# Optimization experiments

Measured on AMD Instinct MI355X. Metric: run time of the kernel, lower is better.

## Reference

```python
import jax, jax.numpy as jnp
import numpy as np

WINDOW = 5
SIGMA = 4.0
KSIZE = 2 * int(4.0 * SIGMA + 0.5) + 1  # 33, matches torchvision GaussianBlur setup

H1, W1, B, N, C = 56, 56, 16, 32, 512
PAD = WINDOW - 1


def _gauss_kernel():
    x = jnp.arange(KSIZE, dtype=jnp.float32) - (KSIZE - 1) / 2.0
    k = jnp.exp(-0.5 * (x / SIGMA) ** 2)
    return k / jnp.sum(k)


def _blur(img):
    # separable Gaussian blur with reflect padding (torchvision GaussianBlur default)
    k = _gauss_kernel()
    p = KSIZE // 2
    x = jnp.pad(img, ((0, 0), (0, 0), (p, p), (p, p)), mode='reflect')
    dn = ('NCHW', 'OIHW', 'NCHW')
    x = jax.lax.conv_general_dilated(x, k.reshape(1, 1, KSIZE, 1), (1, 1), 'VALID', dimension_numbers=dn)
    x = jax.lax.conv_general_dilated(x, k.reshape(1, 1, 1, KSIZE), (1, 1), 'VALID', dimension_numbers=dn)
    return x


def _forward(embeddings, memory_bank, out_h, out_w):
    H, W, Bb, Cc = embeddings.shape
    x_norm = jnp.sum(embeddings * embeddings, axis=-1, keepdims=True)  # H W B 1
    best = None
    for d1 in range(WINDOW):
        for d2 in range(WINDOW):
            y = memory_bank[d1:H + d1, d2:W + d2]            # H W N C (shifted slice)
            y_norm = jnp.sum(y * y, axis=-1)                  # H W N
            cross = jnp.einsum('hwbc,hwnc->hwbn', embeddings, y)
            dsq = jnp.maximum(x_norm - 2.0 * cross + y_norm[:, :, None, :], 0.0)
            dmin = jnp.sqrt(jnp.min(dsq, axis=-1))            # H W B
            best = dmin if best is None else jnp.minimum(best, dmin)
    pix = jnp.transpose(best, (2, 0, 1))[:, None, :, :]        # B 1 H W
    img = jnp.max(pix, axis=(1, 2, 3))                         # B
    pix = jax.image.resize(pix, (Bb, 1, out_h, out_w), method='linear')  # align_corners=False bilinear
    return img, _blur(pix)


def setup_inputs() -> dict:
    key = jax.random.key(0)
    k1, k2 = jax.random.split(key)
    embeddings = jax.random.normal(k1, (H1, W1, B, C), dtype=jnp.float32)
    memory_bank = jax.random.normal(k2, (H1 + PAD, W1 + PAD, N, C), dtype=jnp.float32)
    return {'embeddings': embeddings, 'memory_bank': memory_bank, 'out_h': 224, 'out_w': 224}


def reference(embeddings, memory_bank, out_h, out_w):
    return _forward(embeddings, memory_bank, out_h, out_w)
```

## Files before the change

### kernel.cpp

```cpp
#include <hip/hip_runtime.h>
#include <math.h>

#define H1 56
#define W1 56
#define BB 16
#define NN 32
#define CC 512
#define MH 60
#define MW 60
#define OH 224
#define OW 224

typedef __bf16 bf16x8 __attribute__((ext_vector_type(8)));
typedef float floatx4 __attribute__((ext_vector_type(4)));

#define MBH_OFF    0
#define F_YN_OFF   29491200
#define F_BEST_OFF 29606400
#define F_TMP1_OFF 29656576
#define F_TOTAL_FLOATS 29857280ull

#define S_XN_OFF   0
#define S_YN_OFF   50176
#define S_BEST_OFF 165376
#define S_TMP1_OFF 215552

#define GLOAD_LDS16(g, l) __builtin_amdgcn_global_load_lds( \
    (const __attribute__((address_space(1))) unsigned int*)(g), \
    (__attribute__((address_space(3))) unsigned int*)(l), 16, 0, 0)

__global__ void cvt_norm_kernel(const float* __restrict__ src, __bf16* __restrict__ dsth,
                                float* __restrict__ norm, int nvec) {
    int wid  = (int)((blockIdx.x * blockDim.x + threadIdx.x) >> 6);
    int lane = threadIdx.x & 63;
    if (wid >= nvec) return;
    const float* p = src + (size_t)wid * CC + lane * 8;
    floatx4 a = *(const floatx4*)p;
    floatx4 b = *(const floatx4*)(p + 4);
    if (dsth) {
        bf16x8 v;
        v[0] = (__bf16)a.x; v[1] = (__bf16)a.y; v[2] = (__bf16)a.z; v[3] = (__bf16)a.w;
        v[4] = (__bf16)b.x; v[5] = (__bf16)b.y; v[6] = (__bf16)b.z; v[7] = (__bf16)b.w;
        *(bf16x8*)(dsth + (size_t)wid * CC + lane * 8) = v;
    }
    float s = a.x*a.x + a.y*a.y + a.z*a.z + a.w*a.w
            + b.x*b.x + b.y*b.y + b.z*b.z + b.w*b.w;
    s += __shfl_xor(s, 32, 64);
    s += __shfl_xor(s, 16, 64);
    s += __shfl_xor(s, 8, 64);
    s += __shfl_xor(s, 4, 64);
    s += __shfl_xor(s, 2, 64);
    s += __shfl_xor(s, 1, 64);
    if (lane == 0) norm[wid] = s;
}

#define BSTRIDE 520

__global__ __launch_bounds__(256, 2) void dist_kernel_bf16(
        const float* __restrict__ emb, const __bf16* __restrict__ mbh,
        const float* __restrict__ ynorm, float* __restrict__ best) {
    __shared__ __bf16 Bs[2][NN * BSTRIDE];

    int bx0  = blockIdx.x;
    int bx   = (bx0 & 7) * 49 + (bx0 >> 3);
    int h0   = (bx / 14) * 2;
    int w0   = (bx % 14) * 4;
    int tid  = threadIdx.x;
    int wave = tid >> 6;
    int lane = tid & 63;
    int nrow = lane & 15;
    int seg  = lane >> 4;
    int w    = w0 + wave;

    bf16x8 afragA[16], afragB[16];
    float snA = 0.f, snB = 0.f;
    const float* apA = emb + ((size_t)(h0 * W1 + w) * BB + nrow) * CC + seg * 8;
    const float* apB = apA + (size_t)W1 * BB * CC;
#pragma unroll
    for (int kk = 0; kk < 16; kk++) {
        floatx4 a0 = *(const floatx4*)(apA + kk * 32);
        floatx4 a1 = *(const floatx4*)(apA + kk * 32 + 4);
        floatx4 b0 = *(const floatx4*)(apB + kk * 32);
        floatx4 b1 = *(const floatx4*)(apB + kk * 32 + 4);
        bf16x8 va, vb;
        va[0] = (__bf16)a0.x; va[1] = (__bf16)a0.y; va[2] = (__bf16)a0.z; va[3] = (__bf16)a0.w;
        va[4] = (__bf16)a1.x; va[5] = (__bf16)a1.y; va[6] = (__bf16)a1.z; va[7] = (__bf16)a1.w;
        vb[0] = (__bf16)b0.x; vb[1] = (__bf16)b0.y; vb[2] = (__bf16)b0.z; vb[3] = (__bf16)b0.w;
        vb[4] = (__bf16)b1.x; vb[5] = (__bf16)b1.y; vb[6] = (__bf16)b1.z; vb[7] = (__bf16)b1.w;
        afragA[kk] = va; afragB[kk] = vb;
        snA += a0.x*a0.x + a0.y*a0.y + a0.z*a0.z + a0.w*a0.w
             + a1.x*a1.x + a1.y*a1.y + a1.z*a1.z + a1.w*a1.w;
        snB += b0.x*b0.x + b0.y*b0.y + b0.z*b0.z + b0.w*b0.w
             + b1.x*b1.x + b1.y*b1.y + b1.z*b1.z + b1.w*b1.w;
    }
    snA += __shfl_xor(snA, 16, 64); snA += __shfl_xor(snA, 32, 64);
    snB += __shfl_xor(snB, 16, 64); snB += __shfl_xor(snB, 32, 64);
    floatx4 xnA, xnB;
#pragma unroll
    for (int r = 0; r < 4; r++) {
        xnA[r] = __shfl(snA, seg * 4 + r, 64);
        xnB[r] = __shfl(snB, seg * 4 + r, 64);
    }

    float bvA[4] = {1e30f, 1e30f, 1e30f, 1e30f};
    float bvB[4] = {1e30f, 1e30f, 1e30f, 1e30f};

    {
        const __bf16* bp = mbh + (size_t)(h0 * MW + w0) * NN * CC;
#pragma unroll
        for (int t = 0; t < 8; t++) {
            int n = t * 4 + wave;
            GLOAD_LDS16(bp + (size_t)n * CC + lane * 8, &Bs[0][n * BSTRIDE]);
        }
    }
    __syncthreads();

    int sidx = 0;
    for (int rr = 0; rr < 6; rr++) {
        int mr = h0 + rr;
        for (int j = 0; j < 8; j++, sidx++) {
            int cur = sidx & 1;
            if (sidx + 1 < 48) {
                int nrr = rr + ((j + 1) >> 3);
                int nj  = (j + 1) & 7;
                const __bf16* bp = mbh + (size_t)((h0 + nrr) * MW + (w0 + nj)) * NN * CC;
#pragma unroll
                for (int t = 0; t < 8; t++) {
                    int n = t * 4 + wave;
                    GLOAD_LDS16(bp + (size_t)n * CC + lane * 8, &Bs[cur ^ 1][n * BSTRIDE]);
                }
            }

            int mc = w0 + j;
            int d2 = j - wave;
            if (d2 >= 0 && d2 < 5) {
                const __bf16* Bc = &Bs[cur][0];
                bool a0 = (rr < 5);
                bool a1 = (rr >= 1);
                float yn0 = ynorm[(size_t)(mr * MW + mc) * NN + nrow];
                float yn1 = ynorm[(size_t)(mr * MW + mc) * NN + nrow + 16];
                if (a0 && a1) {
                    floatx4 c0 = {0,0,0,0}, c1 = {0,0,0,0}, c2 = {0,0,0,0}, c3 = {0,0,0,0};
#pragma unroll
                    for (int kk = 0; kk < 16; kk++) {
                        bf16x8 b0 = *(const bf16x8*)(Bc + nrow * BSTRIDE + kk * 32 + seg * 8);
                        bf16x8 b1 = *(const bf16x8*)(Bc + (nrow + 16) * BSTRIDE + kk * 32 + seg * 8);
                        c0 = __builtin_amdgcn_mfma_f32_16x16x32_bf16(afragA[kk], b0, c0, 0, 0, 0);
                        c1 = __builtin_amdgcn_mfma_f32_16x16x32_bf16(afragA[kk], b1, c1, 0, 0, 0);
                        c2 = __builtin_amdgcn_mfma_f32_16x16x32_bf16(afragB[kk], b0, c2, 0, 0, 0);
                        c3 = __builtin_amdgcn_mfma_f32_16x16x32_bf16(afragB[kk], b1, c3, 0, 0, 0);
                    }
#pragma unroll
                    for (int r = 0; r < 4; r++) {
                        bvA[r] = fminf(bvA[r], fminf(fmaxf(xnA[r] - 2.f * c0[r] + yn0, 0.f),
                                                     fmaxf(xnA[r] - 2.f * c1[r] + yn1, 0.f)));
                        bvB[r] = fminf(bvB[r], fminf(fmaxf(xnB[r] - 2.f * c2[r] + yn0, 0.f),
                                                     fmaxf(xnB[r] - 2.f * c3[r] + yn1, 0.f)));
                    }
                } else if (a0) {
                    floatx4 c0 = {0,0,0,0}, c1 = {0,0,0,0};
#pragma unroll
                    for (int kk = 0; kk < 16; kk++) {
                        bf16x8 b0 = *(const bf16x8*)(Bc + nrow * BSTRIDE + kk * 32 + seg * 8);
                        bf16x8 b1 = *(const bf16x8*)(Bc + (nrow + 16) * BSTRIDE + kk * 32 + seg * 8);
                        c0 = __builtin_amdgcn_mfma_f32_16x16x32_bf16(afragA[kk], b0, c0, 0, 0, 0);
                        c1 = __builtin_amdgcn_mfma_f32_16x16x32_bf16(afragA[kk], b1, c1, 0, 0, 0);
                    }
#pragma unroll
                    for (int r = 0; r < 4; r++)
                        bvA[r] = fminf(bvA[r], fminf(fmaxf(xnA[r] - 2.f * c0[r] + yn0, 0.f),
                                                     fmaxf(xnA[r] - 2.f * c1[r] + yn1, 0.f)));
                } else {
                    floatx4 c2 = {0,0,0,0}, c3 = {0,0,0,0};
#pragma unroll
                    for (int kk = 0; kk < 16; kk++) {
                        bf16x8 b0 = *(const bf16x8*)(Bc + nrow * BSTRIDE + kk * 32 + seg * 8);
                        bf16x8 b1 = *(const bf16x8*)(Bc + (nrow + 16) * BSTRIDE + kk * 32 + seg * 8);
                        c2 = __builtin_amdgcn_mfma_f32_16x16x32_bf16(afragB[kk], b0, c2, 0, 0, 0);
                        c3 = __builtin_amdgcn_mfma_f32_16x16x32_bf16(afragB[kk], b1, c3, 0, 0, 0);
                    }
#pragma unroll
                    for (int r = 0; r < 4; r++)
                        bvB[r] = fminf(bvB[r], fminf(fmaxf(xnB[r] - 2.f * c2[r] + yn0, 0.f),
                                                     fmaxf(xnB[r] - 2.f * c3[r] + yn1, 0.f)));
                }
            }
            __syncthreads();
        }
    }

#pragma unroll
    for (int r = 0; r < 4; r++) {
        float v = bvA[r];
        v = fminf(v, __shfl_xor(v, 1, 64));
        v = fminf(v, __shfl_xor(v, 2, 64));
        v = fminf(v, __shfl_xor(v, 4, 64));
        v = fminf(v, __shfl_xor(v, 8, 64));
        bvA[r] = v;
        float u = bvB[r];
        u = fminf(u, __shfl_xor(u, 1, 64));
        u = fminf(u, __shfl_xor(u, 2, 64));
        u = fminf(u, __shfl_xor(u, 4, 64));
        u = fminf(u, __shfl_xor(u, 8, 64));
        bvB[r] = u;
    }
    if ((lane & 15) == 0) {
        int posA = h0 * W1 + w;
        int posB = (h0 + 1) * W1 + w;
#pragma unroll
        for (int r = 0; r < 4; r++) {
            int b = seg * 4 + r;
            best[(size_t)b * (H1 * W1) + posA] = sqrtf(bvA[r]);
            best[(size_t)b * (H1 * W1) + posB] = sqrtf(bvB[r]);
        }
    }
}

__global__ __launch_bounds__(256) void dist_kernel_f32(
        const float* __restrict__ emb, const float* __restrict__ mb,
        const float* __restrict__ xnorm, const float* __restrict__ ynorm,
        float* __restrict__ best) {
    __shared__ __bf16 Bs[NN * BSTRIDE];
    int bx   = blockIdx.x;
    int h    = bx / 14;
    int w0   = (bx % 14) * 4;
    int tid  = threadIdx.x;
    int wave = tid >> 6;
    int lane = tid & 63;
    int nrow = lane & 15;
    int seg  = lane >> 4;
    int w    = w0 + wave;

    bf16x8 afrag[16];
    const float* ap = emb + ((size_t)(h * W1 + w) * BB + nrow) * CC + seg * 8;
#pragma unroll
    for (int kk = 0; kk < 16; kk++) {
        floatx4 f0 = *(const floatx4*)(ap + kk * 32);
        floatx4 f1 = *(const floatx4*)(ap + kk * 32 + 4);
        bf16x8 v;
        v[0] = (__bf16)f0.x; v[1] = (__bf16)f0.y; v[2] = (__bf16)f0.z; v[3] = (__bf16)f0.w;
        v[4] = (__bf16)f1.x; v[5] = (__bf16)f1.y; v[6] = (__bf16)f1.z; v[7] = (__bf16)f1.w;
        afrag[kk] = v;
    }
    floatx4 xn = *(const floatx4*)(xnorm + (size_t)(h * W1 + w) * BB + seg * 4);
    float bestv[4] = {1e30f, 1e30f, 1e30f, 1e30f};

    for (int d1 = 0; d1 < 5; d1++) {
        int mr = h + d1;
        for (int j = 0; j < 8; j++) {
            int mc = w0 + j;
            const float* bp = mb + (size_t)(mr * MW + mc) * NN * CC;
            __syncthreads();
#pragma unroll
            for (int t = 0; t < 8; t++) {
                int c0 = t * 256 + tid;
                int n  = c0 >> 6;
                int ks = (c0 & 63) << 3;
                floatx4 f0 = *(const floatx4*)(bp + n * CC + ks);
                floatx4 f1 = *(const floatx4*)(bp + n * CC + ks + 4);
                bf16x8 v;
                v[0] = (__bf16)f0.x; v[1] = (__bf16)f0.y; v[2] = (__bf16)f0.z; v[3] = (__bf16)f0.w;
                v[4] = (__bf16)f1.x; v[5] = (__bf16)f1.y; v[6] = (__bf16)f1.z; v[7] = (__bf16)f1.w;
                *(bf16x8*)(&Bs[n * BSTRIDE + ks]) = v;
            }
            __syncthreads();

            int d2 = j - wave;
            if (d2 >= 0 && d2 < 5) {
                float yn0 = ynorm[(size_t)(mr * MW + mc) * NN + nrow];
                float yn1 = ynorm[(size_t)(mr * MW + mc) * NN + nrow + 16];
                floatx4 acc0 = {0,0,0,0};
                floatx4 acc1 = {0,0,0,0};
#pragma unroll
                for (int kk = 0; kk < 16; kk++) {
                    bf16x8 b0 = *(const bf16x8*)(&Bs[nrow * BSTRIDE + kk * 32 + seg * 8]);
                    bf16x8 b1 = *(const bf16x8*)(&Bs[(nrow + 16) * BSTRIDE + kk * 32 + seg * 8]);
                    acc0 = __builtin_amdgcn_mfma_f32_16x16x32_bf16(afrag[kk], b0, acc0, 0, 0, 0);
                    acc1 = __builtin_amdgcn_mfma_f32_16x16x32_bf16(afrag[kk], b1, acc1, 0, 0, 0);
                }
#pragma unroll
                for (int r = 0; r < 4; r++) {
                    float d0  = fmaxf(xn[r] - 2.f * acc0[r] + yn0, 0.f);
                    float d1v = fmaxf(xn[r] - 2.f * acc1[r] + yn1, 0.f);
                    bestv[r] = fminf(bestv[r], fminf(d0, d1v));
                }
            }
        }
    }
#pragma unroll
    for (int r = 0; r < 4; r++) {
        float v = bestv[r];
        v = fminf(v, __shfl_xor(v, 1, 64));
        v = fminf(v, __shfl_xor(v, 2, 64));
        v = fminf(v, __shfl_xor(v, 4, 64));
        v = fminf(v, __shfl_xor(v, 8, 64));
        bestv[r] = v;
    }
    if ((lane & 15) == 0) {
        int pos = h * W1 + w;
#pragma unroll
        for (int r = 0; r < 4; r++) {
            int b = seg * 4 + r;
            best[(size_t)b * (H1 * W1) + pos] = sqrtf(bestv[r]);
        }
    }
}

__global__ void max_kernel(const float* __restrict__ best, float* __restrict__ out) {
    __shared__ float red[256];
    int b = blockIdx.x;
    float m = 0.f;
    for (int i = threadIdx.x; i < H1 * W1; i += 256)
        m = fmaxf(m, best[(size_t)b * (H1 * W1) + i]);
    red[threadIdx.x] = m;
    __syncthreads();
    for (int s = 128; s > 0; s >>= 1) {
        if (threadIdx.x < s) red[threadIdx.x] = fmaxf(red[threadIdx.x], red[threadIdx.x + s]);
        __syncthreads();
    }
    if (threadIdx.x == 0) out[b] = red[0];
}

struct GaussK { float k[33]; };

__device__ __forceinline__ int refl(int i, int n) {
    i = (i < 0) ? -i : i;
    i = (i > n - 1) ? 2 * (n - 1) - i : i;
    return i;
}

__global__ void vblur_kernel(const float* __restrict__ best, float* __restrict__ tmp1, GaussK g) {
    int idx = blockIdx.x * 256 + threadIdx.x;
    int lx = idx % W1;
    int y  = (idx / W1) % OH;
    int b  = idx / (W1 * OH);
    const float* p = best + (size_t)b * (H1 * W1);
    float acc = 0.f;
#pragma unroll
    for (int u = 0; u < 33; u++) {
        int z  = refl(y - 16 + u, OH);
        int rz = z & 3;
        float t = 0.125f + 0.25f * (float)((rz + 2) & 3);
        int lo = (z >> 2) + ((rz < 2) ? -1 : 0);
        int hi = min(lo + 1, H1 - 1);
        lo = max(lo, 0);
        acc += g.k[u] * ((1.f - t) * p[lo * W1 + lx] + t * p[hi * W1 + lx]);
    }
    tmp1[idx] = acc;
}

__global__ void hblur_kernel(const float* __restrict__ tmp1, float* __restrict__ dst, GaussK g) {
    int idx = blockIdx.x * 256 + threadIdx.x;
    int x = idx % OW;
    int y = (idx / OW) % OH;
    int b = idx / (OW * OH);
    const float* p = tmp1 + ((size_t)b * OH + y) * W1;
    float acc = 0.f;
#pragma unroll
    for (int u = 0; u < 33; u++) {
        int z  = refl(x - 16 + u, OW);
        int rz = z & 3;
        float t = 0.125f + 0.25f * (float)((rz + 2) & 3);
        int lo = (z >> 2) + ((rz < 2) ? -1 : 0);
        int hi = min(lo + 1, W1 - 1);
        lo = max(lo, 0);
        acc += g.k[u] * ((1.f - t) * p[lo] + t * p[hi]);
    }
    dst[idx] = acc;
}

extern "C" void kernel_launch(void* const* d_in, const int* in_sizes, int n_in,
                              void* d_out, int out_size, void* d_ws, size_t ws_size,
                              hipStream_t stream) {
    const float* emb = (const float*)d_in[0];
    const float* mbp = (const float*)d_in[1];
    float* ws  = (float*)d_ws;
    float* out = (float*)d_out;

    bool big = ws_size >= F_TOTAL_FLOATS * 4ull;

    float* best;
    float* tmp1;

    if (big) {
        __bf16* mbh  = (__bf16*)(ws + MBH_OFF);
        float* ynorm = ws + F_YN_OFF;
        best = ws + F_BEST_OFF;
        tmp1 = ws + F_TMP1_OFF;
        cvt_norm_kernel<<<(MH * MW * NN) / 4, 256, 0, stream>>>(mbp, mbh, ynorm, MH * MW * NN);
        dist_kernel_bf16<<<28 * 14, 256, 0, stream>>>(emb, mbh, ynorm, best);
    } else {
        float* xnorm = ws + S_XN_OFF;
        float* ynorm = ws + S_YN_OFF;
        best = ws + S_BEST_OFF;
        tmp1 = ws + S_TMP1_OFF;
        cvt_norm_kernel<<<(H1 * W1 * BB) / 4, 256, 0, stream>>>(emb, nullptr, xnorm, H1 * W1 * BB);
        cvt_norm_kernel<<<(MH * MW * NN) / 4, 256, 0, stream>>>(mbp, nullptr, ynorm, MH * MW * NN);
        dist_kernel_f32<<<H1 * 14, 256, 0, stream>>>(emb, mbp, xnorm, ynorm, best);
    }

    max_kernel<<<BB, 256, 0, stream>>>(best, out);

    GaussK g;
    {
        double wsum = 0.0, wd[33];
        for (int u = 0; u < 33; u++) {
            double xk = (u - 16) / 4.0;
            wd[u] = exp(-0.5 * xk * xk);
            wsum += wd[u];
        }
        for (int u = 0; u < 33; u++) g.k[u] = (float)(wd[u] / wsum);
    }
    vblur_kernel<<<(BB * OH * W1) / 256, 256, 0, stream>>>(best, tmp1, g);
    hblur_kernel<<<(BB * OH * OW) / 256, 256, 0, stream>>>(tmp1, out + 16, g);
}
```

Before: 492.7 us.

## Widen dist kernel tile to 8 columns with triple-buffered LDS pipeline

```diff
diff --git a/kernel.cpp b/kernel.cpp
--- a/kernel.cpp
+++ b/kernel.cpp
@@ -55,16 +55,21 @@
 }
 
 #define BSTRIDE 520
-
-__global__ __launch_bounds__(256, 2) void dist_kernel_bf16(
+#define NJ 12
+#define NR 6
+#define NSTAGE (NR * NJ)
+
+__global__ __launch_bounds__(512, 2) void dist_kernel_bf16(
         const float* __restrict__ emb, const __bf16* __restrict__ mbh,
         const float* __restrict__ ynorm, float* __restrict__ best) {
-    __shared__ __bf16 Bs[2][NN * BSTRIDE];
+    __shared__ __bf16 Bs[3][NN * BSTRIDE];
+    __shared__ float Ys[NR * NJ * NN];
 
     int bx0  = blockIdx.x;
-    int bx   = (bx0 & 7) * 49 + (bx0 >> 3);
-    int h0   = (bx / 14) * 2;
-    int w0   = (bx % 14) * 4;
+    int xcd  = bx0 & 7, boff = bx0 >> 3;
+    int bx   = (xcd < 4 ? xcd * 25 : 100 + (xcd - 4) * 24) + boff;
+    int h0   = (bx / 7) * 2;
+    int w0   = (bx % 7) * 8;
     int tid  = threadIdx.x;
     int wave = tid >> 6;
     int lane = tid & 63;
@@ -102,43 +107,60 @@
         xnB[r] = __shfl(snB, seg * 4 + r, 64);
     }
 
+    for (int idx = tid; idx < NR * NJ * NN; idx += 512) {
+        int row = idx / (NJ * NN);
+        int c   = idx - row * (NJ * NN);
+        Ys[idx] = ynorm[((size_t)((h0 + row) * MW + w0)) * NN + c];
+    }
+
     float bvA[4] = {1e30f, 1e30f, 1e30f, 1e30f};
     float bvB[4] = {1e30f, 1e30f, 1e30f, 1e30f};
 
-    {
-        const __bf16* bp = mbh + (size_t)(h0 * MW + w0) * NN * CC;
-#pragma unroll
-        for (int t = 0; t < 8; t++) {
-            int n = t * 4 + wave;
-            GLOAD_LDS16(bp + (size_t)n * CC + lane * 8, &Bs[0][n * BSTRIDE]);
-        }
-    }
-    __syncthreads();
-
+#pragma unroll
+    for (int s = 0; s < 2; s++) {
+        const __bf16* bp = mbh + (size_t)(h0 * MW + (w0 + s)) * NN * CC;
+#pragma unroll
+        for (int t = 0; t < 4; t++) {
+            int n = wave * 4 + t;
+            GLOAD_LDS16(bp + (size_t)n * CC + lane * 8, &Bs[s][n * BSTRIDE]);
+        }
+    }
+    asm volatile("s_waitcnt lgkmcnt(0)" ::: "memory");
+
+    int rd = 0;
     int sidx = 0;
-    for (int rr = 0; rr < 6; rr++) {
+    for (int rr = 0; rr < NR; rr++) {
         int mr = h0 + rr;
-        for (int j = 0; j < 8; j++, sidx++) {
-            int cur = sidx & 1;
-            if (sidx + 1 < 48) {
-                int nrr = rr + ((j + 1) >> 3);
-                int nj  = (j + 1) & 7;
-                const __bf16* bp = mbh + (size_t)((h0 + nrr) * MW + (w0 + nj)) * NN * CC;
-#pragma unroll
-                for (int t = 0; t < 8; t++) {
-                    int n = t * 4 + wave;
-                    GLOAD_LDS16(bp + (size_t)n * CC + lane * 8, &Bs[cur ^ 1][n * BSTRIDE]);
+        for (int j = 0; j < NJ; j++, sidx++) {
+            __builtin_amdgcn_sched_barrier(0);
+            if (sidx < NSTAGE - 1) {
+                asm volatile("s_waitcnt vmcnt(4)" ::: "memory");
+            } else {
+                asm volatile("s_waitcnt vmcnt(0)" ::: "memory");
+            }
+            __builtin_amdgcn_sched_barrier(0);
+            __builtin_amdgcn_s_barrier();
+
+            if (sidx + 2 < NSTAGE) {
+                int j2  = j + 2;
+                int rr2 = rr + (j2 >= NJ ? 1 : 0);
+                j2 -= (j2 >= NJ ? NJ : 0);
+                int wr = rd + 2; if (wr >= 3) wr -= 3;
+                const __bf16* bp = mbh + (size_t)((h0 + rr2) * MW + (w0 + j2)) * NN * CC;
+#pragma unroll
+                for (int t = 0; t < 4; t++) {
+                    int n = wave * 4 + t;
+                    GLOAD_LDS16(bp + (size_t)n * CC + lane * 8, &Bs[wr][n * BSTRIDE]);
                 }
             }
 
-            int mc = w0 + j;
             int d2 = j - wave;
             if (d2 >= 0 && d2 < 5) {
-                const __bf16* Bc = &Bs[cur][0];
+                const __bf16* Bc = &Bs[rd][0];
                 bool a0 = (rr < 5);
                 bool a1 = (rr >= 1);
-                float yn0 = ynorm[(size_t)(mr * MW + mc) * NN + nrow];
-                float yn1 = ynorm[(size_t)(mr * MW + mc) * NN + nrow + 16];
+                float yn0 = Ys[(rr * NJ + j) * NN + nrow];
+                float yn1 = Ys[(rr * NJ + j) * NN + nrow + 16];
                 if (a0 && a1) {
                     floatx4 c0 = {0,0,0,0}, c1 = {0,0,0,0}, c2 = {0,0,0,0}, c3 = {0,0,0,0};
 #pragma unroll
@@ -185,7 +207,7 @@
                                                      fmaxf(xnB[r] - 2.f * c3[r] + yn1, 0.f)));
                 }
             }
-            __syncthreads();
+            rd++; if (rd >= 3) rd = 0;
         }
     }
 
@@ -388,7 +410,7 @@
         best = ws + F_BEST_OFF;
         tmp1 = ws + F_TMP1_OFF;
         cvt_norm_kernel<<<(MH * MW * NN) / 4, 256, 0, stream>>>(mbp, mbh, ynorm, MH * MW * NN);
-        dist_kernel_bf16<<<28 * 14, 256, 0, stream>>>(emb, mbh, ynorm, best);
+        dist_kernel_bf16<<<28 * 7, 512, 0, stream>>>(emb, mbh, ynorm, best);
     } else {
         float* xnorm = ws + S_XN_OFF;
         float* ynorm = ws + S_YN_OFF;
```

Measured after the change: 541.8 us. 1.1x slower.

## Split memory-bank tiles into half-row stages with a 4-deep async LDS pipeline

Applied to the files above, without the earlier changes.

```diff
diff --git a/kernel.cpp b/kernel.cpp
--- a/kernel.cpp
+++ b/kernel.cpp
@@ -55,11 +55,14 @@
 }
 
 #define BSTRIDE 520
+#define HROWS 16
+#define NHS (6 * 8 * 2)
 
 __global__ __launch_bounds__(256, 2) void dist_kernel_bf16(
         const float* __restrict__ emb, const __bf16* __restrict__ mbh,
         const float* __restrict__ ynorm, float* __restrict__ best) {
-    __shared__ __bf16 Bs[2][NN * BSTRIDE];
+    __shared__ __bf16 Bs[4][HROWS * BSTRIDE];
+    __shared__ float Ys[6 * 8 * NN];
 
     int bx0  = blockIdx.x;
     int bx   = (bx0 & 7) * 49 + (bx0 >> 3);
@@ -102,90 +105,86 @@
         xnB[r] = __shfl(snB, seg * 4 + r, 64);
     }
 
+    for (int idx = tid; idx < 6 * 8 * NN; idx += 256) {
+        int row = idx >> 8;
+        int c   = idx & 255;
+        Ys[idx] = ynorm[((size_t)((h0 + row) * MW + w0)) * NN + c];
+    }
+
     float bvA[4] = {1e30f, 1e30f, 1e30f, 1e30f};
     float bvB[4] = {1e30f, 1e30f, 1e30f, 1e30f};
 
-    {
-        const __bf16* bp = mbh + (size_t)(h0 * MW + w0) * NN * CC;
-#pragma unroll
-        for (int t = 0; t < 8; t++) {
-            int n = t * 4 + wave;
-            GLOAD_LDS16(bp + (size_t)n * CC + lane * 8, &Bs[0][n * BSTRIDE]);
-        }
-    }
-    __syncthreads();
+#pragma unroll
+    for (int t = 0; t < 3; t++) {
+        int p  = t >> 1;
+        int hh = t & 1;
+        const __bf16* bp = mbh + ((size_t)((h0 + (p >> 3)) * MW + (w0 + (p & 7))) * NN
+                                  + hh * HROWS) * CC;
+#pragma unroll
+        for (int tt = 0; tt < 4; tt++) {
+            int n = wave * 4 + tt;
+            GLOAD_LDS16(bp + (size_t)n * CC + lane * 8, &Bs[t][n * BSTRIDE]);
+        }
+    }
+    asm volatile("s_waitcnt lgkmcnt(0)" ::: "memory");
 
     int sidx = 0;
     for (int rr = 0; rr < 6; rr++) {
-        int mr = h0 + rr;
-        for (int j = 0; j < 8; j++, sidx++) {
-            int cur = sidx & 1;
-            if (sidx + 1 < 48) {
-                int nrr = rr + ((j + 1) >> 3);
-                int nj  = (j + 1) & 7;
-                const __bf16* bp = mbh + (size_t)((h0 + nrr) * MW + (w0 + nj)) * NN * CC;
-#pragma unroll
-                for (int t = 0; t < 8; t++) {
-                    int n = t * 4 + wave;
-                    GLOAD_LDS16(bp + (size_t)n * CC + lane * 8, &Bs[cur ^ 1][n * BSTRIDE]);
+        bool a0 = (rr < 5);
+        bool a1 = (rr >= 1);
+        for (int j = 0; j < 8; j++) {
+            int d2 = j - wave;
+            bool act = (d2 >= 0 && d2 < 5);
+            const float* yrow = &Ys[(rr * 8 + j) * NN];
+#pragma unroll
+            for (int hh = 0; hh < 2; hh++, sidx++) {
+                int slot = sidx & 3;
+                __builtin_amdgcn_sched_barrier(0);
+                if (sidx < NHS - 2) {
+                    asm volatile("s_waitcnt vmcnt(8)" ::: "memory");
+                } else if (sidx == NHS - 2) {
+                    asm volatile("s_waitcnt vmcnt(4)" ::: "memory");
+                } else {
+                    asm volatile("s_waitcnt vmcnt(0)" ::: "memory");
+                }
+                __builtin_amdgcn_sched_barrier(0);
+                __builtin_amdgcn_s_barrier();
+
+                int t3 = sidx + 3;
+                if (t3 < NHS) {
+                    int p3  = t3 >> 1;
+                    int hh3 = t3 & 1;
+                    const __bf16* bp = mbh + ((size_t)((h0 + (p3 >> 4)) * MW
+                                          + (w0 + ((p3 >> 1) & 7))) * NN + hh3 * HROWS) * CC;
+#pragma unroll
+                    for (int tt = 0; tt < 4; tt++) {
+                        int n = wave * 4 + tt;
+                        GLOAD_LDS16(bp + (size_t)n * CC + lane * 8, &Bs[t3 & 3][n * BSTRIDE]);
+                    }
+                }
+
+                if (act) {
+                    const __bf16* Bc = &Bs[slot][0];
+                    float yn = yrow[nrow + hh * 16];
+                    floatx4 cA = {0,0,0,0}, cB = {0,0,0,0};
+#pragma unroll
+                    for (int kk = 0; kk < 16; kk++) {
+                        bf16x8 b = *(const bf16x8*)(Bc + nrow * BSTRIDE + kk * 32 + seg * 8);
+                        cA = __builtin_amdgcn_mfma_f32_16x16x32_bf16(afragA[kk], b, cA, 0, 0, 0);
+                        cB = __builtin_amdgcn_mfma_f32_16x16x32_bf16(afragB[kk], b, cB, 0, 0, 0);
+                    }
+                    if (a0) {
+#pragma unroll
+                        for (int r = 0; r < 4; r++)
+                            bvA[r] = fminf(bvA[r], fmaxf(xnA[r] - 2.f * cA[r] + yn, 0.f));
+                    }
+                    if (a1) {
+#pragma unroll
+                        for (int r = 0; r < 4; r++)
+                            bvB[r] = fminf(bvB[r], fmaxf(xnB[r] - 2.f * cB[r] + yn, 0.f));
+                    }
                 }
             }
-
-            int mc = w0 + j;
-            int d2 = j - wave;
-            if (d2 >= 0 && d2 < 5) {
-                const __bf16* Bc = &Bs[cur][0];
-                bool a0 = (rr < 5);
-                bool a1 = (rr >= 1);
-                float yn0 = ynorm[(size_t)(mr * MW + mc) * NN + nrow];
-                float yn1 = ynorm[(size_t)(mr * MW + mc) * NN + nrow + 16];
-                if (a0 && a1) {
-                    floatx4 c0 = {0,0,0,0}, c1 = {0,0,0,0}, c2 = {0,0,0,0}, c3 = {0,0,0,0};
-#pragma unroll
-                    for (int kk = 0; kk < 16; kk++) {
-                        bf16x8 b0 = *(const bf16x8*)(Bc + nrow * BSTRIDE + kk * 32 + seg * 8);
-                        bf16x8 b1 = *(const bf16x8*)(Bc + (nrow + 16) * BSTRIDE + kk * 32 + seg * 8);
-                        c0 = __builtin_amdgcn_mfma_f32_16x16x32_bf16(afragA[kk], b0, c0, 0, 0, 0);
-                        c1 = __builtin_amdgcn_mfma_f32_16x16x32_bf16(afragA[kk], b1, c1, 0, 0, 0);
-                        c2 = __builtin_amdgcn_mfma_f32_16x16x32_bf16(afragB[kk], b0, c2, 0, 0, 0);
-                        c3 = __builtin_amdgcn_mfma_f32_16x16x32_bf16(afragB[kk], b1, c3, 0, 0, 0);
-                    }
-#pragma unroll
-                    for (int r = 0; r < 4; r++) {
-                        bvA[r] = fminf(bvA[r], fminf(fmaxf(xnA[r] - 2.f * c0[r] + yn0, 0.f),
-                                                     fmaxf(xnA[r] - 2.f * c1[r] + yn1, 0.f)));
-                        bvB[r] = fminf(bvB[r], fminf(fmaxf(xnB[r] - 2.f * c2[r] + yn0, 0.f),
-                                                     fmaxf(xnB[r] - 2.f * c3[r] + yn1, 0.f)));
-                    }
-                } else if (a0) {
-                    floatx4 c0 = {0,0,0,0}, c1 = {0,0,0,0};
-#pragma unroll
-                    for (int kk = 0; kk < 16; kk++) {
-                        bf16x8 b0 = *(const bf16x8*)(Bc + nrow * BSTRIDE + kk * 32 + seg * 8);
-                        bf16x8 b1 = *(const bf16x8*)(Bc + (nrow + 16) * BSTRIDE + kk * 32 + seg * 8);
-                        c0 = __builtin_amdgcn_mfma_f32_16x16x32_bf16(afragA[kk], b0, c0, 0, 0, 0);
-                        c1 = __builtin_amdgcn_mfma_f32_16x16x32_bf16(afragA[kk], b1, c1, 0, 0, 0);
-                    }
-#pragma unroll
-                    for (int r = 0; r < 4; r++)
-                        bvA[r] = fminf(bvA[r], fminf(fmaxf(xnA[r] - 2.f * c0[r] + yn0, 0.f),
-                                                     fmaxf(xnA[r] - 2.f * c1[r] + yn1, 0.f)));
-                } else {
-                    floatx4 c2 = {0,0,0,0}, c3 = {0,0,0,0};
-#pragma unroll
-                    for (int kk = 0; kk < 16; kk++) {
-                        bf16x8 b0 = *(const bf16x8*)(Bc + nrow * BSTRIDE + kk * 32 + seg * 8);
-                        bf16x8 b1 = *(const bf16x8*)(Bc + (nrow + 16) * BSTRIDE + kk * 32 + seg * 8);
-                        c2 = __builtin_amdgcn_mfma_f32_16x16x32_bf16(afragB[kk], b0, c2, 0, 0, 0);
-                        c3 = __builtin_amdgcn_mfma_f32_16x16x32_bf16(afragB[kk], b1, c3, 0, 0, 0);
-                    }
-#pragma unroll
-                    for (int r = 0; r < 4; r++)
-                        bvB[r] = fminf(bvB[r], fminf(fmaxf(xnB[r] - 2.f * c2[r] + yn0, 0.f),
-                                                     fmaxf(xnB[r] - 2.f * c3[r] + yn1, 0.f)));
-                }
-            }
-            __syncthreads();
         }
     }
 
```

Measured after the change: 534.8 us. 1.09x slower.
